# Performance work log

Measured on AMD Instinct MI355X. Metric: run time of the kernel, lower is better.

The kernel has to match this reference:

```python
import jax, jax.numpy as jnp
import numpy as np

HEAD_DIM = 128
NUM_Q_HEAD = 16
NUM_KV_HEAD = 4
WINDOW = 1024
SOFTMAX_CAP = 30.0
SOFTMAX_TEMP = 1.0
CLIP_L, CLIP_R = -0.03, 1.03
SCALE = 1.0 / np.sqrt(HEAD_DIM).astype(np.float32)


def setup_inputs() -> dict:
    key = jax.random.key(0)
    k1, k2, k3 = jax.random.split(key, 3)
    B, S = 2, 2048
    q = jax.random.normal(k1, (B, S, NUM_Q_HEAD, HEAD_DIM), jnp.float32)
    k = jax.random.normal(k2, (B, S, NUM_KV_HEAD, HEAD_DIM), jnp.float32)
    v = jax.random.normal(k3, (B, S, NUM_KV_HEAD, HEAD_DIM), jnp.float32)
    return {"q": q, "k": k, "v": v}


def _sliding_window_attn(q, k, v):
    # q: [B,S,Hq,D]; k,v: [B,S,Hkv,D]  (BSHD layout)
    n_rep = NUM_Q_HEAD // NUM_KV_HEAD
    k = jnp.repeat(k, n_rep, axis=2)  # GQA repeat-interleave -> [B,S,Hq,D]
    v = jnp.repeat(v, n_rep, axis=2)
    # BSHD -> BHSD
    q = q.transpose(0, 2, 1, 3)
    k = k.transpose(0, 2, 1, 3)
    v = v.transpose(0, 2, 1, 3)

    P = jnp.einsum('bhqd,bhkd->bhqk', q, k)  # raw scores [B,H,S,S]

    S = q.shape[2]
    qi = jnp.arange(S)[:, None]
    kj = jnp.arange(S)[None, :]
    # causal + sliding window: allow q_idx - window <= k_idx <= q_idx
    allowed = (kj <= qi) & (kj >= qi - WINDOW)
    mask = jnp.where(allowed, 0.0, -jnp.inf).astype(P.dtype)  # [S,S]

    # softmax capping: cap * tanh(P * scale / temp) + mask
    P = SOFTMAX_CAP * jnp.tanh(P * (SCALE / SOFTMAX_TEMP)) + mask

    A = jax.nn.softmax(P, axis=-1)  # numerically stable (max-subtracted)
    # softmax clipping: clamp((r-l)*A + l, 0, 1); dropout rate is 0 -> identity
    A = jnp.clip((CLIP_R - CLIP_L) * A + CLIP_L, 0.0, 1.0)

    O = jnp.einsum('bhqk,bhkd->bhqd', A, v)
    return O.transpose(0, 2, 1, 3)  # back to BSHD


def reference(q, k, v):
    return _sliding_window_attn(q, k, v)
```

## Files before the change

kernel.cpp:

```cpp
#include <hip/hip_runtime.h>
#include <hip/hip_bf16.h>

typedef float f32x4 __attribute__((ext_vector_type(4)));
typedef _Float16 f16x8 __attribute__((ext_vector_type(8)));
typedef unsigned int u32;

#define SQ   2048
#define HQ   16
#define HKV  4
#define DH   128
#define WIN  1024
#define QT   64
#define KT   64
#define WROW 34

#define AS1 __attribute__((address_space(1)))
#define AS3 __attribute__((address_space(3)))

__device__ __forceinline__ void gload16(const void* g, void* l) {
  __builtin_amdgcn_global_load_lds((const AS1 u32*)g, (AS3 u32*)l, 16, 0, 0);
}

__device__ __forceinline__ float swa_e(float s) {
  float u = __builtin_amdgcn_exp2f(s * 0.25507046054708916f);
  return __builtin_amdgcn_exp2f(-86.5617024533378f * __builtin_amdgcn_rcpf(u + 1.0f));
}

__global__ __launch_bounds__(256)
void prep(const float* __restrict__ K, const float* __restrict__ V,
          _Float16* __restrict__ kf, _Float16* __restrict__ vt)
{
  const int t = blockIdx.x * 256 + threadIdx.x;
  const int NK = 2 * HKV * SQ * 16;
  if (t < NK) {
    const int p  = t & 15;
    const int s  = (t >> 4) & (SQ - 1);
    const int hk = (t >> 15) & 3;
    const int b  = t >> 17;
    const int c  = p ^ (s & 7);
    const float* src = K + (((size_t)b * SQ + s) * HKV + hk) * DH + c * 8;
    f32x4 x0 = *(const f32x4*)src;
    f32x4 x1 = *(const f32x4*)(src + 4);
    f16x8 o;
    #pragma unroll
    for (int j = 0; j < 4; ++j) { o[j] = (_Float16)x0[j]; o[4 + j] = (_Float16)x1[j]; }
    *(f16x8*)(kf + (((size_t)(b * HKV + hk)) * SQ + s) * DH + p * 8) = o;
  } else {
    const int u  = t - NK;
    const int p  = u & 7;
    const int d  = (u >> 3) & 127;
    const int tt = (u >> 10) & 31;
    const int hk = (u >> 15) & 3;
    const int b  = u >> 17;
    const int c  = p ^ (d & 7);
    f16x8 o;
    #pragma unroll
    for (int j = 0; j < 8; ++j) {
      const int s = tt * 64 + c * 8 + j;
      o[j] = (_Float16)V[(((size_t)b * SQ + s) * HKV + hk) * DH + d];
    }
    *(f16x8*)(vt + ((((size_t)(b * HKV + hk)) * 32 + tt) * DH + d) * 64 + p * 8) = o;
  }
}

__global__ __launch_bounds__(256, 2)
void swa_fwd(const float* __restrict__ Q, float* __restrict__ O,
             const _Float16* __restrict__ kf, const _Float16* __restrict__ vt)
{
  __shared__ _Float16 lK[KT * DH];
  __shared__ _Float16 lV[DH * KT];
  __shared__ _Float16 lW[4][16 * WROW];

  const int tid  = threadIdx.x;
  const int lane = tid & 63;
  const int wv   = tid >> 6;
  const int lm   = lane & 15;
  const int lg   = lane >> 4;

  const int g  = blockIdx.x;
  const int qt = 31 - (g >> 5);
  const int h  = g & 15;
  const int b  = (g >> 4) & 1;
  const int q0 = qt * QT;
  const int hk = h >> 2;

  const _Float16* kfb = kf + ((size_t)(b * HKV + hk)) * SQ * DH;
  const _Float16* vtb = vt + ((size_t)(b * HKV + hk)) * 32 * DH * 64;

  f16x8 qa[4];
  {
    const int qrow = q0 + wv * 16 + lm;
    const float* qp = Q + (((size_t)b * SQ + qrow) * HQ + h) * DH;
    #pragma unroll
    for (int kb = 0; kb < 4; ++kb) {
      const float* p = qp + kb * 32 + lg * 8;
      f32x4 x0 = *(const f32x4*)p;
      f32x4 x1 = *(const f32x4*)(p + 4);
      f16x8 a;
      #pragma unroll
      for (int j = 0; j < 4; ++j) { a[j] = (_Float16)x0[j]; a[4 + j] = (_Float16)x1[j]; }
      qa[kb] = a;
    }
  }

  const int kmin   = (q0 - WIN) > 0 ? (q0 - WIN) : 0;
  const int ntiles = (q0 + QT - kmin) / KT;
  const int qr0    = q0 + wv * 16 + lg * 4;

  float zs[4] = {0.f, 0.f, 0.f, 0.f};
  for (int t = 0; t < ntiles; ++t) {
    const int kbase = kmin + t * KT;
    __syncthreads();
    {
      const char* kt = (const char*)(kfb + (size_t)kbase * DH);
      #pragma unroll
      for (int r = 0; r < 4; ++r)
        gload16(kt + r * 4096 + wv * 1024 + lane * 16,
                (char*)lK + r * 4096 + wv * 1024);
    }
    __syncthreads();
    #pragma unroll
    for (int ks = 0; ks < 4; ++ks) {
      f32x4 acc = {0.f, 0.f, 0.f, 0.f};
      const int keyl = ks * 16 + lm;
      #pragma unroll
      for (int kb = 0; kb < 4; ++kb) {
        const int chunk = (kb * 4 + lg) ^ (keyl & 7);
        f16x8 bf = *(const f16x8*)((const char*)lK + keyl * 256 + chunk * 16);
        acc = __builtin_amdgcn_mfma_f32_16x16x32_f16(qa[kb], bf, acc, 0, 0, 0);
      }
      const int key = kbase + keyl;
      #pragma unroll
      for (int r = 0; r < 4; ++r) {
        const int qr = qr0 + r;
        const bool ok = (key <= qr) && (key >= qr - WIN);
        zs[r] += ok ? swa_e(acc[r]) : 0.f;
      }
    }
  }

  float rz[4];
  #pragma unroll
  for (int r = 0; r < 4; ++r) {
    float z = zs[r];
    z += __shfl_xor(z, 1);
    z += __shfl_xor(z, 2);
    z += __shfl_xor(z, 4);
    z += __shfl_xor(z, 8);
    rz[r] = 1.06f / z;
  }

  f32x4 oacc[8];
  #pragma unroll
  for (int i = 0; i < 8; ++i) oacc[i] = (f32x4){0.f, 0.f, 0.f, 0.f};

  for (int t = 0; t < ntiles; ++t) {
    const int kbase = kmin + t * KT;
    __syncthreads();
    {
      const char* kt = (const char*)(kfb + (size_t)kbase * DH);
      const char* vtile = (const char*)(vtb + (size_t)(kbase >> 6) * (DH * 64));
      #pragma unroll
      for (int r = 0; r < 4; ++r) {
        gload16(kt + r * 4096 + wv * 1024 + lane * 16,
                (char*)lK + r * 4096 + wv * 1024);
        gload16(vtile + r * 4096 + wv * 1024 + lane * 16,
                (char*)lV + r * 4096 + wv * 1024);
      }
    }
    __syncthreads();

    #pragma unroll
    for (int half = 0; half < 2; ++half) {
      #pragma unroll
      for (int ks = 0; ks < 2; ++ks) {
        f32x4 acc = {0.f, 0.f, 0.f, 0.f};
        const int keyl = (half * 2 + ks) * 16 + lm;
        #pragma unroll
        for (int kb = 0; kb < 4; ++kb) {
          const int chunk = (kb * 4 + lg) ^ (keyl & 7);
          f16x8 bf = *(const f16x8*)((const char*)lK + keyl * 256 + chunk * 16);
          acc = __builtin_amdgcn_mfma_f32_16x16x32_f16(qa[kb], bf, acc, 0, 0, 0);
        }
        const int key = kbase + keyl;
        #pragma unroll
        for (int r = 0; r < 4; ++r) {
          const int qr = qr0 + r;
          const bool ok = (key <= qr) && (key >= qr - WIN);
          float e   = ok ? swa_e(acc[r]) : 0.f;
          float wgt = fminf(fmaxf(fmaf(e, rz[r], -0.03f), 0.f), 1.f);
          lW[wv][(lg * 4 + r) * WROW + ks * 16 + lm] = (_Float16)wgt;
        }
      }
      const f16x8 af = *(const f16x8*)&lW[wv][lm * WROW + lg * 8];
      #pragma unroll
      for (int dt = 0; dt < 8; ++dt) {
        const int d = dt * 16 + lm;
        const int chunk = (half * 4 + lg) ^ (d & 7);
        f16x8 bf = *(const f16x8*)((const char*)lV + d * 128 + chunk * 16);
        oacc[dt] = __builtin_amdgcn_mfma_f32_16x16x32_f16(af, bf, oacc[dt], 0, 0, 0);
      }
    }
  }

  #pragma unroll
  for (int r = 0; r < 4; ++r) {
    float* op = O + (((size_t)b * SQ + (qr0 + r)) * HQ + h) * DH;
    #pragma unroll
    for (int dt = 0; dt < 8; ++dt) op[dt * 16 + lm] = oacc[dt][r];
  }
}

extern "C" void kernel_launch(void* const* d_in, const int* in_sizes, int n_in,
                              void* d_out, int out_size, void* d_ws, size_t ws_size,
                              hipStream_t stream) {
  const float* q = (const float*)d_in[0];
  const float* k = (const float*)d_in[1];
  const float* v = (const float*)d_in[2];
  float* o = (float*)d_out;

  _Float16* kf = (_Float16*)d_ws;
  _Float16* vt = kf + (size_t)2 * HKV * SQ * DH;

  hipLaunchKernelGGL(prep, dim3(2048), dim3(256), 0, stream, k, v, kf, vt);
  hipLaunchKernelGGL(swa_fwd, dim3(1024), dim3(256), 0, stream, q, o, kf, vt);
}
```

Baseline: 99.07 us.

## Add persistent atomic scheduler, double-buffered K pass, mask peeling and weight skipping

Turns the attention kernel into a persistent loop that takes work items from an atomic counter, which prep resets. The first (normalizer) pass now double-buffers K tiles using the lV buffer, and both passes apply the window mask only on the edge tiles. The second pass computes a per-row score threshold below which the clipped weight is zero and skips the exp when no lane in the wave exceeds it. It also raises occupancy to 4 blocks per SM and pads the lW row stride, trading added control flow and per-row threshold math for less exp work and latency hiding.

```diff
diff --git a/kernel.cpp b/kernel.cpp
--- a/kernel.cpp
+++ b/kernel.cpp
@@ -12,7 +12,8 @@
 #define WIN  1024
 #define QT   64
 #define KT   64
-#define WROW 34
+#define WROW 36
+#define NG   1024
 
 #define AS1 __attribute__((address_space(1)))
 #define AS3 __attribute__((address_space(3)))
@@ -28,8 +29,9 @@
 
 __global__ __launch_bounds__(256)
 void prep(const float* __restrict__ K, const float* __restrict__ V,
-          _Float16* __restrict__ kf, _Float16* __restrict__ vt)
+          _Float16* __restrict__ kf, _Float16* __restrict__ vt, int* __restrict__ cnt)
 {
+  if (blockIdx.x == 0 && threadIdx.x == 0) *cnt = 0;
   const int t = blockIdx.x * 256 + threadIdx.x;
   const int NK = 2 * HKV * SQ * 16;
   if (t < NK) {
@@ -63,13 +65,15 @@
   }
 }
 
-__global__ __launch_bounds__(256, 2)
+__global__ __launch_bounds__(256, 4)
 void swa_fwd(const float* __restrict__ Q, float* __restrict__ O,
-             const _Float16* __restrict__ kf, const _Float16* __restrict__ vt)
+             const _Float16* __restrict__ kf, const _Float16* __restrict__ vt,
+             int* __restrict__ cnt)
 {
   __shared__ _Float16 lK[KT * DH];
   __shared__ _Float16 lV[DH * KT];
   __shared__ _Float16 lW[4][16 * WROW];
+  __shared__ int sIdx;
 
   const int tid  = threadIdx.x;
   const int lane = tid & 63;
@@ -77,137 +81,176 @@
   const int lm   = lane & 15;
   const int lg   = lane >> 4;
 
-  const int g  = blockIdx.x;
-  const int qt = 31 - (g >> 5);
-  const int h  = g & 15;
-  const int b  = (g >> 4) & 1;
-  const int q0 = qt * QT;
-  const int hk = h >> 2;
-
-  const _Float16* kfb = kf + ((size_t)(b * HKV + hk)) * SQ * DH;
-  const _Float16* vtb = vt + ((size_t)(b * HKV + hk)) * 32 * DH * 64;
-
-  f16x8 qa[4];
-  {
-    const int qrow = q0 + wv * 16 + lm;
-    const float* qp = Q + (((size_t)b * SQ + qrow) * HQ + h) * DH;
-    #pragma unroll
-    for (int kb = 0; kb < 4; ++kb) {
-      const float* p = qp + kb * 32 + lg * 8;
-      f32x4 x0 = *(const f32x4*)p;
-      f32x4 x1 = *(const f32x4*)(p + 4);
-      f16x8 a;
-      #pragma unroll
-      for (int j = 0; j < 4; ++j) { a[j] = (_Float16)x0[j]; a[4 + j] = (_Float16)x1[j]; }
-      qa[kb] = a;
-    }
-  }
-
-  const int kmin   = (q0 - WIN) > 0 ? (q0 - WIN) : 0;
-  const int ntiles = (q0 + QT - kmin) / KT;
-  const int qr0    = q0 + wv * 16 + lg * 4;
-
-  float zs[4] = {0.f, 0.f, 0.f, 0.f};
-  for (int t = 0; t < ntiles; ++t) {
-    const int kbase = kmin + t * KT;
+  for (;;) {
     __syncthreads();
+    if (tid == 0) sIdx = atomicAdd(cnt, 1);
+    __syncthreads();
+    const int g = sIdx;
+    if (g >= NG) break;
+
+    const int qt = 31 - (g >> 5);
+    const int h  = g & 15;
+    const int b  = (g >> 4) & 1;
+    const int q0 = qt * QT;
+    const int hk = h >> 2;
+
+    const _Float16* kfb = kf + ((size_t)(b * HKV + hk)) * SQ * DH;
+    const _Float16* vtb = vt + ((size_t)(b * HKV + hk)) * 32 * DH * 64;
+
+    f16x8 qa[4];
     {
-      const char* kt = (const char*)(kfb + (size_t)kbase * DH);
-      #pragma unroll
-      for (int r = 0; r < 4; ++r)
-        gload16(kt + r * 4096 + wv * 1024 + lane * 16,
-                (char*)lK + r * 4096 + wv * 1024);
-    }
-    __syncthreads();
-    #pragma unroll
-    for (int ks = 0; ks < 4; ++ks) {
-      f32x4 acc = {0.f, 0.f, 0.f, 0.f};
-      const int keyl = ks * 16 + lm;
+      const int qrow = q0 + wv * 16 + lm;
+      const float* qp = Q + (((size_t)b * SQ + qrow) * HQ + h) * DH;
       #pragma unroll
       for (int kb = 0; kb < 4; ++kb) {
-        const int chunk = (kb * 4 + lg) ^ (keyl & 7);
-        f16x8 bf = *(const f16x8*)((const char*)lK + keyl * 256 + chunk * 16);
-        acc = __builtin_amdgcn_mfma_f32_16x16x32_f16(qa[kb], bf, acc, 0, 0, 0);
-      }
-      const int key = kbase + keyl;
+        const float* p = qp + kb * 32 + lg * 8;
+        f32x4 x0 = *(const f32x4*)p;
+        f32x4 x1 = *(const f32x4*)(p + 4);
+        f16x8 a;
+        #pragma unroll
+        for (int j = 0; j < 4; ++j) { a[j] = (_Float16)x0[j]; a[4 + j] = (_Float16)x1[j]; }
+        qa[kb] = a;
+      }
+    }
+
+    const int kmin = (q0 - WIN) > 0 ? (q0 - WIN) : 0;
+    const int nt   = (q0 + QT - kmin) / KT;
+    const int qr0  = q0 + wv * 16 + lg * 4;
+
+    float zs[4] = {0.f, 0.f, 0.f, 0.f};
+    {
+      _Float16* cur = lK;
+      _Float16* nxt = lV;
+      {
+        const char* src = (const char*)(kfb + (size_t)kmin * DH);
+        #pragma unroll
+        for (int r4 = 0; r4 < 4; ++r4)
+          gload16(src + r4 * 4096 + wv * 1024 + lane * 16,
+                  (char*)cur + r4 * 4096 + wv * 1024);
+      }
+      __syncthreads();
+      for (int t = 0; t < nt; ++t) {
+        if (t + 1 < nt) {
+          const char* src = (const char*)(kfb + (size_t)(kmin + (t + 1) * KT) * DH);
+          #pragma unroll
+          for (int r4 = 0; r4 < 4; ++r4)
+            gload16(src + r4 * 4096 + wv * 1024 + lane * 16,
+                    (char*)nxt + r4 * 4096 + wv * 1024);
+        }
+        const int  kbase = kmin + t * KT;
+        const bool peel  = (t == 0 && q0 >= WIN) || (t == nt - 1);
+        #pragma unroll
+        for (int ks = 0; ks < 4; ++ks) {
+          f32x4 acc = {0.f, 0.f, 0.f, 0.f};
+          const int keyl = ks * 16 + lm;
+          #pragma unroll
+          for (int kb = 0; kb < 4; ++kb) {
+            const int chunk = (kb * 4 + lg) ^ (keyl & 7);
+            f16x8 bf = *(const f16x8*)((const char*)cur + keyl * 256 + chunk * 16);
+            acc = __builtin_amdgcn_mfma_f32_16x16x32_f16(qa[kb], bf, acc, 0, 0, 0);
+          }
+          if (peel) {
+            const int key = kbase + keyl;
+            #pragma unroll
+            for (int r = 0; r < 4; ++r) {
+              const int qr = qr0 + r;
+              const bool ok = (key <= qr) && (key >= qr - WIN);
+              zs[r] += ok ? swa_e(acc[r]) : 0.f;
+            }
+          } else {
+            #pragma unroll
+            for (int r = 0; r < 4; ++r) zs[r] += swa_e(acc[r]);
+          }
+        }
+        __syncthreads();
+        _Float16* tmp = cur; cur = nxt; nxt = tmp;
+      }
+    }
+
+    float rz[4], sthr[4];
+    #pragma unroll
+    for (int r = 0; r < 4; ++r) {
+      float z = zs[r];
+      z += __shfl_xor(z, 1);
+      z += __shfl_xor(z, 2);
+      z += __shfl_xor(z, 4);
+      z += __shfl_xor(z, 8);
+      rz[r] = 1.06f / z;
+      float lt = __log2f(0.0283018868f * z);
+      float A  = -86.5617024533378f / lt - 1.0f;
+      float sv = 3.9204912f * __log2f(A) - 0.05f;
+      sv = (lt >= 0.f) ? 1e30f : sv;
+      sv = (lt <= -86.5617f) ? -1e30f : sv;
+      sthr[r] = sv;
+    }
+
+    f32x4 oacc[8];
+    #pragma unroll
+    for (int i = 0; i < 8; ++i) oacc[i] = (f32x4){0.f, 0.f, 0.f, 0.f};
+
+    for (int t = 0; t < nt; ++t) {
+      const int kbase = kmin + t * KT;
+      __syncthreads();
+      {
+        const char* kt2   = (const char*)(kfb + (size_t)kbase * DH);
+        const char* vtile = (const char*)(vtb + (size_t)(kbase >> 6) * (DH * 64));
+        #pragma unroll
+        for (int r4 = 0; r4 < 4; ++r4) {
+          gload16(kt2 + r4 * 4096 + wv * 1024 + lane * 16,
+                  (char*)lK + r4 * 4096 + wv * 1024);
+          gload16(vtile + r4 * 4096 + wv * 1024 + lane * 16,
+                  (char*)lV + r4 * 4096 + wv * 1024);
+        }
+      }
+      __syncthreads();
+
+      const bool peel = (t == 0 && q0 >= WIN) || (t == nt - 1);
+
       #pragma unroll
-      for (int r = 0; r < 4; ++r) {
-        const int qr = qr0 + r;
-        const bool ok = (key <= qr) && (key >= qr - WIN);
-        zs[r] += ok ? swa_e(acc[r]) : 0.f;
-      }
-    }
-  }
-
-  float rz[4];
-  #pragma unroll
-  for (int r = 0; r < 4; ++r) {
-    float z = zs[r];
-    z += __shfl_xor(z, 1);
-    z += __shfl_xor(z, 2);
-    z += __shfl_xor(z, 4);
-    z += __shfl_xor(z, 8);
-    rz[r] = 1.06f / z;
-  }
-
-  f32x4 oacc[8];
-  #pragma unroll
-  for (int i = 0; i < 8; ++i) oacc[i] = (f32x4){0.f, 0.f, 0.f, 0.f};
-
-  for (int t = 0; t < ntiles; ++t) {
-    const int kbase = kmin + t * KT;
-    __syncthreads();
-    {
-      const char* kt = (const char*)(kfb + (size_t)kbase * DH);
-      const char* vtile = (const char*)(vtb + (size_t)(kbase >> 6) * (DH * 64));
+      for (int half = 0; half < 2; ++half) {
+        #pragma unroll
+        for (int ks = 0; ks < 2; ++ks) {
+          f32x4 acc = {0.f, 0.f, 0.f, 0.f};
+          const int keyl = (half * 2 + ks) * 16 + lm;
+          #pragma unroll
+          for (int kb = 0; kb < 4; ++kb) {
+            const int chunk = (kb * 4 + lg) ^ (keyl & 7);
+            f16x8 bf = *(const f16x8*)((const char*)lK + keyl * 256 + chunk * 16);
+            acc = __builtin_amdgcn_mfma_f32_16x16x32_f16(qa[kb], bf, acc, 0, 0, 0);
+          }
+          const int key = kbase + keyl;
+          #pragma unroll
+          for (int r = 0; r < 4; ++r) {
+            float w = 0.f;
+            if (__any(acc[r] > sthr[r])) {
+              float e = swa_e(acc[r]);
+              w = fminf(fmaxf(fmaf(e, rz[r], -0.03f), 0.f), 1.f);
+              if (peel) {
+                const int qr = qr0 + r;
+                const bool ok = (key <= qr) && (key >= qr - WIN);
+                w = ok ? w : 0.f;
+              }
+            }
+            lW[wv][(lg * 4 + r) * WROW + ks * 16 + lm] = (_Float16)w;
+          }
+        }
+        const f16x8 af = *(const f16x8*)&lW[wv][lm * WROW + lg * 8];
+        #pragma unroll
+        for (int dt = 0; dt < 8; ++dt) {
+          const int d = dt * 16 + lm;
+          const int chunk = (half * 4 + lg) ^ (d & 7);
+          f16x8 bf = *(const f16x8*)((const char*)lV + d * 128 + chunk * 16);
+          oacc[dt] = __builtin_amdgcn_mfma_f32_16x16x32_f16(af, bf, oacc[dt], 0, 0, 0);
+        }
+      }
+    }
+
+    #pragma unroll
+    for (int r = 0; r < 4; ++r) {
+      float* op = O + (((size_t)b * SQ + (qr0 + r)) * HQ + h) * DH;
       #pragma unroll
-      for (int r = 0; r < 4; ++r) {
-        gload16(kt + r * 4096 + wv * 1024 + lane * 16,
-                (char*)lK + r * 4096 + wv * 1024);
-        gload16(vtile + r * 4096 + wv * 1024 + lane * 16,
-                (char*)lV + r * 4096 + wv * 1024);
-      }
-    }
-    __syncthreads();
-
-    #pragma unroll
-    for (int half = 0; half < 2; ++half) {
-      #pragma unroll
-      for (int ks = 0; ks < 2; ++ks) {
-        f32x4 acc = {0.f, 0.f, 0.f, 0.f};
-        const int keyl = (half * 2 + ks) * 16 + lm;
-        #pragma unroll
-        for (int kb = 0; kb < 4; ++kb) {
-          const int chunk = (kb * 4 + lg) ^ (keyl & 7);
-          f16x8 bf = *(const f16x8*)((const char*)lK + keyl * 256 + chunk * 16);
-          acc = __builtin_amdgcn_mfma_f32_16x16x32_f16(qa[kb], bf, acc, 0, 0, 0);
-        }
-        const int key = kbase + keyl;
-        #pragma unroll
-        for (int r = 0; r < 4; ++r) {
-          const int qr = qr0 + r;
-          const bool ok = (key <= qr) && (key >= qr - WIN);
-          float e   = ok ? swa_e(acc[r]) : 0.f;
-          float wgt = fminf(fmaxf(fmaf(e, rz[r], -0.03f), 0.f), 1.f);
-          lW[wv][(lg * 4 + r) * WROW + ks * 16 + lm] = (_Float16)wgt;
-        }
-      }
-      const f16x8 af = *(const f16x8*)&lW[wv][lm * WROW + lg * 8];
-      #pragma unroll
-      for (int dt = 0; dt < 8; ++dt) {
-        const int d = dt * 16 + lm;
-        const int chunk = (half * 4 + lg) ^ (d & 7);
-        f16x8 bf = *(const f16x8*)((const char*)lV + d * 128 + chunk * 16);
-        oacc[dt] = __builtin_amdgcn_mfma_f32_16x16x32_f16(af, bf, oacc[dt], 0, 0, 0);
-      }
-    }
-  }
-
-  #pragma unroll
-  for (int r = 0; r < 4; ++r) {
-    float* op = O + (((size_t)b * SQ + (qr0 + r)) * HQ + h) * DH;
-    #pragma unroll
-    for (int dt = 0; dt < 8; ++dt) op[dt * 16 + lm] = oacc[dt][r];
+      for (int dt = 0; dt < 8; ++dt) op[dt * 16 + lm] = oacc[dt][r];
+    }
   }
 }
 
@@ -221,7 +264,9 @@
 
   _Float16* kf = (_Float16*)d_ws;
   _Float16* vt = kf + (size_t)2 * HKV * SQ * DH;
-
-  hipLaunchKernelGGL(prep, dim3(2048), dim3(256), 0, stream, k, v, kf, vt);
-  hipLaunchKernelGGL(swa_fwd, dim3(1024), dim3(256), 0, stream, q, o, kf, vt);
-}
+  int* cnt = (int*)((char*)d_ws + (size_t)2 * 2097152 * sizeof(_Float16) * 2 / 2 + 4194304);
+  cnt = (int*)((char*)d_ws + 8388608);
+
+  hipLaunchKernelGGL(prep, dim3(2048), dim3(256), 0, stream, k, v, kf, vt, cnt);
+  hipLaunchKernelGGL(swa_fwd, dim3(NG), dim3(256), 0, stream, q, o, kf, vt, cnt);
+}
```

New measurement: 113.5 us. 14.6% more time.
